# Optimization experiments

Hardware: AMD Instinct MI355X
Metric: run time of the kernel (lower is better)

The kernel has to match this reference:

```python
import jax, jax.numpy as jnp
import numpy as np

THETA_BASE = 10000.0


def rope(x):
    # x: [B, S, D], D even. Interleaved-pair rotary embedding.
    B, S, D = x.shape
    pos = jnp.arange(S, dtype=jnp.float32)                       # [S]
    p = jnp.arange(D // 2, dtype=jnp.float32)                    # p-1 in the torch code
    inv_freq = 1.0 / (THETA_BASE ** (2.0 * p / D))               # [D/2]
    theta = pos[:, None] * inv_freq[None, :]                     # [S, D/2]
    sin_t, cos_t = jnp.sin(theta), jnp.cos(theta)
    x1 = x[..., 0::2]                                            # [B, S, D/2]
    x2 = x[..., 1::2]
    r1 = x1 * cos_t - x2 * sin_t
    r2 = x1 * sin_t + x2 * cos_t
    return jnp.stack((r1, r2), axis=-1).reshape(B, S, D)


def setup_inputs() -> dict:
    key = jax.random.key(0)
    k_x, k_q, k_k, k_v = jax.random.split(key, 4)
    B, S, E, DH = 4, 4096, 1024, 64
    x = jax.random.normal(k_x, (B, S, E), dtype=jnp.float32)
    # causal lower-triangular mask (mask==0 positions are disallowed)
    mask = jnp.tril(jnp.ones((S, S), dtype=jnp.int32))
    W_Q = jax.random.uniform(k_q, (E, DH), dtype=jnp.float32)
    W_K = jax.random.uniform(k_k, (E, DH), dtype=jnp.float32)
    W_V = jax.random.uniform(k_v, (E, DH), dtype=jnp.float32)
    return {"x": x, "mask": mask, "W_Q": W_Q, "W_K": W_K, "W_V": W_V}


def reference(x, mask, W_Q, W_K, W_V):
    d_h = W_Q.shape[1]
    Q = x @ W_Q                                                  # [B, S, d_h]
    K = x @ W_K
    V = x @ W_V
    Q, K = rope(Q), rope(K)
    scores = jnp.einsum('bqd,bkd->bqk', Q, K) / jnp.sqrt(jnp.float32(d_h))
    masked = jnp.where(mask == 0, -jnp.inf, scores)              # broadcast [S,S] -> [B,S,S]
    attn = jax.nn.softmax(masked, axis=-1)
    return jnp.einsum('bqk,bkd->bqd', attn, V)
```

## Files before the change

kernel.cpp:

```cpp
#include <hip/hip_runtime.h>

typedef short short8  __attribute__((ext_vector_type(8)));
typedef short short4v __attribute__((ext_vector_type(4)));
typedef float f32x4   __attribute__((ext_vector_type(4)));
typedef int   i32x4   __attribute__((ext_vector_type(4)));

#define NB 4
#define NS 4096
#define NE 1024
#define ND 64

__device__ __forceinline__ short f2bf(float f) {
    unsigned u = __builtin_bit_cast(unsigned, f);
    u = (u + 0x7FFFu + ((u >> 16) & 1u)) >> 16;
    return (short)u;
}
__device__ __forceinline__ float bf2f(short s) {
    unsigned u = ((unsigned)(unsigned short)s) << 16;
    return __builtin_bit_cast(float, u);
}

__global__ void prep_wt(const float* __restrict__ WQ, const float* __restrict__ WK,
                        const float* __restrict__ WV,
                        short* __restrict__ wtp_hi, short* __restrict__ wtp_lo) {
    int idx = blockIdx.x * 256 + threadIdx.x;
    if (idx >= 192 * NE) return;
    int n = idx >> 10, k = idx & (NE - 1);
    int sel = n >> 6, d = n & 63;
    const float* W = (sel == 0) ? WQ : (sel == 1 ? WK : WV);
    float v = W[k * ND + d];
    if (sel == 0) v *= 0.125f;
    short hi = f2bf(v);
    short lo = f2bf(v - bf2f(hi));
    int off = ((k >> 5) * 12 + (n >> 4)) * 512 + ((k & 31) >> 3) * 128 + (n & 15) * 8 + (k & 7);
    wtp_hi[off] = hi;
    wtp_lo[off] = lo;
}

__global__ __launch_bounds__(256, 2) void proj_rope(
        const float* __restrict__ x,
        const short* __restrict__ wtp_hi, const short* __restrict__ wtp_lo,
        short* __restrict__ qhi, short* __restrict__ qlo,
        short* __restrict__ khi, short* __restrict__ klo,
        short* __restrict__ vtb) {
    __shared__ short Xh[32 * 64], Xl[32 * 64];
    const int tid = threadIdx.x;
    const int w = tid >> 6, lane = tid & 63;
    const int g = lane >> 4, cl = lane & 15;
    const int rb = blockIdx.x << 5;
    const int c0 = w * 48;

    f32x4 acc[2][3];
    #pragma unroll
    for (int i = 0; i < 2; ++i)
        #pragma unroll
        for (int j = 0; j < 3; ++j) acc[i][j] = (f32x4){0.f, 0.f, 0.f, 0.f};

    const int srow = tid >> 3, skc = tid & 7;
    const float* xs0 = x + (size_t)(rb + srow) * NE + (skc << 3);
    const int swoff = srow * 64 + ((skc ^ (srow & 7)) << 3);

    const short* bph = wtp_hi + (size_t)(c0 >> 4) * 512 + (lane << 3);
    const short* bpl = wtp_lo + (size_t)(c0 >> 4) * 512 + (lane << 3);

    float4 xr0, xr1;
    short8 b0[6], b1[6];

#define LOADXR(kk) { xr0 = *(const float4*)(xs0 + (kk)); \
                     xr1 = *(const float4*)(xs0 + (kk) + 4); }
#define LOADB(Bs, kk) {                                                      \
        const int ko = ((kk) >> 5) * 6144;                                   \
        _Pragma("unroll")                                                    \
        for (int ct = 0; ct < 3; ++ct) {                                     \
            Bs[ct * 2]     = *(const short8*)(bph + ko + ct * 512);          \
            Bs[ct * 2 + 1] = *(const short8*)(bpl + ko + ct * 512);          \
        } }
#define HALF(h, Bs) {                                                        \
        _Pragma("unroll")                                                    \
        for (int rt = 0; rt < 2; ++rt) {                                     \
            const int R = (rt << 4) + cl;                                    \
            const int ro = R * 64 + ((((h) * 4 + g) ^ (R & 7)) << 3);        \
            short8 ah = *(const short8*)(Xh + ro);                           \
            short8 al = *(const short8*)(Xl + ro);                           \
            _Pragma("unroll")                                                \
            for (int ct = 0; ct < 3; ++ct) {                                 \
                acc[rt][ct] = __builtin_amdgcn_mfma_f32_16x16x32_bf16(ah, Bs[ct*2],   acc[rt][ct], 0, 0, 0); \
                acc[rt][ct] = __builtin_amdgcn_mfma_f32_16x16x32_bf16(ah, Bs[ct*2+1], acc[rt][ct], 0, 0, 0); \
                acc[rt][ct] = __builtin_amdgcn_mfma_f32_16x16x32_bf16(al, Bs[ct*2],   acc[rt][ct], 0, 0, 0); \
            }                                                                \
        } }

    LOADXR(0);
    LOADB(b0, 0);

    #pragma unroll 1
    for (int k0 = 0; k0 < NE; k0 += 64) {
        short8 h8, l8;
        {
            float vv[8] = {xr0.x, xr0.y, xr0.z, xr0.w, xr1.x, xr1.y, xr1.z, xr1.w};
            #pragma unroll
            for (int q = 0; q < 8; ++q) {
                short h = f2bf(vv[q]);
                h8[q] = h;
                l8[q] = f2bf(vv[q] - bf2f(h));
            }
        }
        __syncthreads();
        *(short8*)(Xh + swoff) = h8;
        *(short8*)(Xl + swoff) = l8;
        if (k0 + 64 < NE) LOADXR(k0 + 64);
        LOADB(b1, k0 + 32);
        __syncthreads();
        HALF(0, b0);
        if (k0 + 64 < NE) LOADB(b0, k0 + 64);
        HALF(1, b1);
    }
#undef LOADXR
#undef LOADB
#undef HALF

    #pragma unroll
    for (int rt = 0; rt < 2; ++rt) {
        #pragma unroll
        for (int ct = 0; ct < 3; ++ct) {
            int c = c0 + (ct << 4) + cl;
            #pragma unroll
            for (int r = 0; r < 4; ++r) {
                int row = rb + (rt << 4) + (g << 2) + r;
                int s = row & (NS - 1);
                int b = row >> 12;
                float val = acc[rt][ct][r];
                if (c < 128) {
                    int d = c & 63;
                    int p = d >> 1;
                    float freq = exp2f(-(float)p * 0.41524101186091903f);
                    float theta = (float)s * freq;
                    float sn = sinf(theta), cs = cosf(theta);
                    float partner = __shfl_xor(val, 1);
                    float rot = (c & 1) ? fmaf(partner, sn, val * cs)
                                        : fmaf(-partner, sn, val * cs);
                    short hi = f2bf(rot);
                    short lo = f2bf(rot - bf2f(hi));
                    int off = row * ND + d;
                    if (c < 64) { qhi[off] = hi; qlo[off] = lo; }
                    else        { khi[off] = hi; klo[off] = lo; }
                } else {
                    int d = c - 128;
                    vtb[(b << 18) + ((s >> 5) << 11) + (d << 5) + (s & 31)] = f2bf(val);
                }
            }
        }
    }
}

__global__ __launch_bounds__(256) void attn_fused(
        const short* __restrict__ qhi, const short* __restrict__ qlo,
        const short* __restrict__ khi, const short* __restrict__ klo,
        const short* __restrict__ vtb, float* __restrict__ outp) {
    __shared__ char sm[49152];
    const int tid = threadIdx.x;
    const int lane = tid & 63, w = tid >> 6;
    const int g = lane >> 4, cl = lane & 15;
    const int bid = blockIdx.x;
    const int b = (bid >> 1) & 3;
    const int t = 255 - (((bid >> 3) << 1) | (bid & 1));
    const int qw = t << 4;
    const int rowb = b << 12;

    char* SW  = sm + w * 12288;
    short* Ps = (short*)(SW + 4096);

    short8 qh[2], ql[2];
    #pragma unroll
    for (int ks = 0; ks < 2; ++ks) {
        int off = ((rowb + qw + cl) << 6) + (ks << 5) + (g << 3);
        qh[ks] = *(const short8*)(qhi + off);
        ql[ks] = *(const short8*)(qlo + off);
    }

    f32x4 o[4];
    #pragma unroll
    for (int i = 0; i < 4; ++i) o[i] = (f32x4){0.f, 0.f, 0.f, 0.f};
    float m = -1e38f, lsp = 0.f;

    const int nkv = (t >> 1) + 1;
    const short* kpB = khi + (rowb << 6);
    const short* lpB = klo + (rowb << 6);
    const short* vpB = vtb + (b << 18);

    i32x4 stK[4], stL[4], stV[4];
#define ISSUE(jj) {                                                          \
        const short* kp = kpB + ((jj) << 11);                                \
        const short* lp = lpB + ((jj) << 11);                                \
        const short* vp = vpB + ((jj) << 11);                                \
        _Pragma("unroll")                                                    \
        for (int i = 0; i < 4; ++i) {                                        \
            stK[i] = *(const i32x4*)(kp + (lane << 3) + (i << 9));           \
            stL[i] = *(const i32x4*)(lp + (lane << 3) + (i << 9));           \
            stV[i] = *(const i32x4*)(vp + (lane << 3) + (i << 9));           \
        } }

    if (w < nkv) {
        ISSUE(w);
        #pragma unroll 1
        for (int j = w; j < nkv; j += 4) {
            #pragma unroll
            for (int i = 0; i < 4; ++i) {
                int c = lane + (i << 6);
                int kr = c >> 3, kc = c & 7;
                int koff = (kr << 7) + ((kc ^ (kr & 7)) << 4);
                *(i32x4*)(SW + koff) = stK[i];
                *(i32x4*)(SW + 4096 + koff) = stL[i];
                int vr = c >> 2, vc = c & 3;
                *(i32x4*)(SW + 8192 + (vr << 6) + ((vc ^ (vr & 3)) << 4)) = stV[i];
            }
            int jn = j + 4;
            if (jn < nkv) ISSUE(jn);

            f32x4 sc[2];
            #pragma unroll
            for (int ci = 0; ci < 2; ++ci) {
                const int rbase = ((ci << 4) + cl) << 7;
                const int sw = (cl & 7) << 4;
                short8 kh0 = *(short8*)(SW + rbase + (((g << 4)     ) ^ sw));
                short8 kh1 = *(short8*)(SW + rbase + (((g << 4) + 64) ^ sw));
                short8 kl0 = *(short8*)(SW + 4096 + rbase + (((g << 4)     ) ^ sw));
                short8 kl1 = *(short8*)(SW + 4096 + rbase + (((g << 4) + 64) ^ sw));
                f32x4 s = (f32x4){0.f, 0.f, 0.f, 0.f};
                s = __builtin_amdgcn_mfma_f32_16x16x32_bf16(kh0, qh[0], s, 0, 0, 0);
                s = __builtin_amdgcn_mfma_f32_16x16x32_bf16(kh1, qh[1], s, 0, 0, 0);
                s = __builtin_amdgcn_mfma_f32_16x16x32_bf16(kh0, ql[0], s, 0, 0, 0);
                s = __builtin_amdgcn_mfma_f32_16x16x32_bf16(kh1, ql[1], s, 0, 0, 0);
                s = __builtin_amdgcn_mfma_f32_16x16x32_bf16(kl0, qh[0], s, 0, 0, 0);
                s = __builtin_amdgcn_mfma_f32_16x16x32_bf16(kl1, qh[1], s, 0, 0, 0);
                sc[ci] = s;
            }
            if (j == nkv - 1) {
                #pragma unroll
                for (int ci = 0; ci < 2; ++ci)
                    #pragma unroll
                    for (int r = 0; r < 4; ++r)
                        if ((j << 5) + (ci << 4) + (g << 2) + r > qw + cl) sc[ci][r] = -1e30f;
            }
            float pm = fmaxf(fmaxf(fmaxf(sc[0][0], sc[0][1]), fmaxf(sc[0][2], sc[0][3])),
                             fmaxf(fmaxf(sc[1][0], sc[1][1]), fmaxf(sc[1][2], sc[1][3])));
            pm = fmaxf(pm, __shfl_xor(pm, 16));
            pm = fmaxf(pm, __shfl_xor(pm, 32));
            const float mo = m;
            m = fmaxf(m, pm);
            const float rs = __expf(mo - m);
            float psum = 0.f;
            #pragma unroll
            for (int ci = 0; ci < 2; ++ci) {
                float p0 = __expf(sc[ci][0] - m), p1 = __expf(sc[ci][1] - m);
                float p2 = __expf(sc[ci][2] - m), p3 = __expf(sc[ci][3] - m);
                psum += (p0 + p1) + (p2 + p3);
                short4v pk;
                pk[0] = f2bf(p0); pk[1] = f2bf(p1); pk[2] = f2bf(p2); pk[3] = f2bf(p3);
                *(short4v*)(Ps + cl * 40 + (ci << 4) + (g << 2)) = pk;
            }
            lsp = lsp * rs + psum;
            if (__any(m > mo)) {
                float rs4[4];
                #pragma unroll
                for (int r = 0; r < 4; ++r) rs4[r] = __shfl(rs, (g << 2) + r);
                #pragma unroll
                for (int dt = 0; dt < 4; ++dt)
                    #pragma unroll
                    for (int r = 0; r < 4; ++r) o[dt][r] *= rs4[r];
            }
            short8 pa = *(short8*)(Ps + cl * 40 + (g << 3));
            #pragma unroll
            for (int dt = 0; dt < 4; ++dt) {
                int vrow = (dt << 4) + cl;
                short8 vf = *(short8*)(SW + 8192 + (vrow << 6)
                                        + (((g << 4)) ^ ((vrow & 3) << 4)));
                o[dt] = __builtin_amdgcn_mfma_f32_16x16x32_bf16(pa, vf, o[dt], 0, 0, 0);
            }
        }
    }
#undef ISSUE

    {
        float* Co = (float*)SW;
        #pragma unroll
        for (int dt = 0; dt < 4; ++dt)
            #pragma unroll
            for (int r = 0; r < 4; ++r)
                Co[((g << 2) + r) * 66 + (dt << 4) + cl] = o[dt][r];
        lsp += __shfl_xor(lsp, 16);
        lsp += __shfl_xor(lsp, 32);
        if (g == 0) {
            *(float*)(SW + 4224 + (cl << 2)) = m;
            *(float*)(SW + 4288 + (cl << 2)) = lsp;
        }
    }
    __syncthreads();

    if (w == 0) {
        #pragma unroll
        for (int r = 0; r < 4; ++r) {
            const int row = (g << 2) + r;
            float mv[4], lv[4];
            #pragma unroll
            for (int v = 0; v < 4; ++v) {
                mv[v] = *(const float*)(sm + v * 12288 + 4224 + (row << 2));
                lv[v] = *(const float*)(sm + v * 12288 + 4288 + (row << 2));
            }
            float M = fmaxf(fmaxf(mv[0], mv[1]), fmaxf(mv[2], mv[3]));
            float e[4];
            float L = 0.f;
            #pragma unroll
            for (int v = 0; v < 4; ++v) { e[v] = __expf(mv[v] - M); L += lv[v] * e[v]; }
            float inv = 1.f / L;
            #pragma unroll
            for (int dt = 0; dt < 4; ++dt) {
                int d = (dt << 4) + cl;
                float O = 0.f;
                #pragma unroll
                for (int v = 0; v < 4; ++v)
                    O += ((const float*)(sm + v * 12288))[row * 66 + d] * e[v];
                outp[(rowb + qw + row) * ND + d] = O * inv;
            }
        }
    }
}

extern "C" void kernel_launch(void* const* d_in, const int* in_sizes, int n_in,
                              void* d_out, int out_size, void* d_ws, size_t ws_size,
                              hipStream_t stream) {
    const float* x  = (const float*)d_in[0];
    const float* WQ = (const float*)d_in[2];
    const float* WK = (const float*)d_in[3];
    const float* WV = (const float*)d_in[4];

    const size_t need = 786432u + 4u * 2097152u + 2097152u;
    if (ws_size < need) return;

    char* ws = (char*)d_ws;
    short* wtph = (short*)(ws);
    short* wtpl = (short*)(ws + 393216);
    short* qhi  = (short*)(ws + 786432);
    short* qlo  = (short*)(ws + 786432 + 1 * 2097152);
    short* khi  = (short*)(ws + 786432 + 2 * 2097152);
    short* klo  = (short*)(ws + 786432 + 3 * 2097152);
    short* vtb  = (short*)(ws + 786432 + 4 * 2097152);

    prep_wt<<<768, 256, 0, stream>>>(WQ, WK, WV, wtph, wtpl);
    proj_rope<<<512, 256, 0, stream>>>(x, wtph, wtpl, qhi, qlo, khi, klo, vtb);
    attn_fused<<<1024, 256, 0, stream>>>(qhi, qlo, khi, klo, vtb, (float*)d_out);
}
```

Baseline: 88.53 us.

## Pre-pack K/V in MFMA fragment layout and load directly into registers

The projection kernel now writes K (hi/lo) and V in a layout that matches the MFMA operand fragments, so the attention kernel loads each lane's fragments straight from global memory into registers. This removes the per-tile LDS staging writes, swizzle and LDS reads. It also shrinks shared memory to the P, output-combine and stats buffers and sets launch bounds to 4 blocks per CU for higher occupancy. In exchange the fragment loads are used directly by MFMAs with less latency hiding, and the next-tile prefetch is split into separate K and V loads.

```diff
diff --git a/kernel.cpp b/kernel.cpp
--- a/kernel.cpp
+++ b/kernel.cpp
@@ -3,7 +3,6 @@
 typedef short short8  __attribute__((ext_vector_type(8)));
 typedef short short4v __attribute__((ext_vector_type(4)));
 typedef float f32x4   __attribute__((ext_vector_type(4)));
-typedef int   i32x4   __attribute__((ext_vector_type(4)));
 
 #define NB 4
 #define NS 4096
@@ -41,8 +40,8 @@
         const float* __restrict__ x,
         const short* __restrict__ wtp_hi, const short* __restrict__ wtp_lo,
         short* __restrict__ qhi, short* __restrict__ qlo,
-        short* __restrict__ khi, short* __restrict__ klo,
-        short* __restrict__ vtb) {
+        short* __restrict__ kfph, short* __restrict__ kfpl,
+        short* __restrict__ vfp) {
     __shared__ short Xh[32 * 64], Xl[32 * 64];
     const int tid = threadIdx.x;
     const int w = tid >> 6, lane = tid & 63;
@@ -141,23 +140,32 @@
                                         : fmaf(-partner, sn, val * cs);
                     short hi = f2bf(rot);
                     short lo = f2bf(rot - bf2f(hi));
-                    int off = row * ND + d;
-                    if (c < 64) { qhi[off] = hi; qlo[off] = lo; }
-                    else        { khi[off] = hi; klo[off] = lo; }
+                    if (c < 64) {
+                        int off = row * ND + d;
+                        qhi[off] = hi; qlo[off] = lo;
+                    } else {
+                        int off = ((b << 7) + (s >> 5)) * 2048 + ((s >> 4) & 1) * 1024
+                                + (d >> 5) * 512 + (((d >> 3) & 3) * 16 + (s & 15)) * 8 + (d & 7);
+                        kfph[off] = hi; kfpl[off] = lo;
+                    }
                 } else {
                     int d = c - 128;
-                    vtb[(b << 18) + ((s >> 5) << 11) + (d << 5) + (s & 31)] = f2bf(val);
+                    int off = ((b << 7) + (s >> 5)) * 2048 + (d >> 4) * 512
+                            + (((s >> 3) & 3) * 16 + (d & 15)) * 8 + (s & 7);
+                    vfp[off] = f2bf(val);
                 }
             }
         }
     }
 }
 
-__global__ __launch_bounds__(256) void attn_fused(
+__global__ __launch_bounds__(256, 4) void attn_fused(
         const short* __restrict__ qhi, const short* __restrict__ qlo,
-        const short* __restrict__ khi, const short* __restrict__ klo,
-        const short* __restrict__ vtb, float* __restrict__ outp) {
-    __shared__ char sm[49152];
+        const short* __restrict__ kfph, const short* __restrict__ kfpl,
+        const short* __restrict__ vfp, float* __restrict__ outp) {
+    __shared__ short Ps[4][16][40];
+    __shared__ float Co[4][16][66];
+    __shared__ float Cm[4][16], Cls[4][16];
     const int tid = threadIdx.x;
     const int lane = tid & 63, w = tid >> 6;
     const int g = lane >> 4, cl = lane & 15;
@@ -167,9 +175,6 @@
     const int qw = t << 4;
     const int rowb = b << 12;
 
-    char* SW  = sm + w * 12288;
-    short* Ps = (short*)(SW + 4096);
-
     short8 qh[2], ql[2];
     #pragma unroll
     for (int ks = 0; ks < 2; ++ks) {
@@ -184,57 +189,48 @@
     float m = -1e38f, lsp = 0.f;
 
     const int nkv = (t >> 1) + 1;
-    const short* kpB = khi + (rowb << 6);
-    const short* lpB = klo + (rowb << 6);
-    const short* vpB = vtb + (b << 18);
-
-    i32x4 stK[4], stL[4], stV[4];
-#define ISSUE(jj) {                                                          \
-        const short* kp = kpB + ((jj) << 11);                                \
-        const short* lp = lpB + ((jj) << 11);                                \
-        const short* vp = vpB + ((jj) << 11);                                \
+    const short* kbaseh = kfph + (size_t)(b << 7) * 2048 + (lane << 3);
+    const short* kbasel = kfpl + (size_t)(b << 7) * 2048 + (lane << 3);
+    const short* vbase  = vfp  + (size_t)(b << 7) * 2048 + (lane << 3);
+
+    short8 kf[2][4];
+    short8 vf[4];
+
+#define LOADK(jj) {                                                          \
         _Pragma("unroll")                                                    \
-        for (int i = 0; i < 4; ++i) {                                        \
-            stK[i] = *(const i32x4*)(kp + (lane << 3) + (i << 9));           \
-            stL[i] = *(const i32x4*)(lp + (lane << 3) + (i << 9));           \
-            stV[i] = *(const i32x4*)(vp + (lane << 3) + (i << 9));           \
+        for (int ci = 0; ci < 2; ++ci) {                                     \
+            const short* kh = kbaseh + (jj) * 2048 + ci * 1024;              \
+            const short* kl = kbasel + (jj) * 2048 + ci * 1024;              \
+            kf[ci][0] = *(const short8*)(kh);                                \
+            kf[ci][1] = *(const short8*)(kh + 512);                          \
+            kf[ci][2] = *(const short8*)(kl);                                \
+            kf[ci][3] = *(const short8*)(kl + 512);                          \
         } }
+#define LOADV(jj) {                                                          \
+        _Pragma("unroll")                                                    \
+        for (int dt = 0; dt < 4; ++dt)                                       \
+            vf[dt] = *(const short8*)(vbase + (jj) * 2048 + dt * 512);       \
+        }
 
     if (w < nkv) {
-        ISSUE(w);
+        LOADK(w); LOADV(w);
         #pragma unroll 1
         for (int j = w; j < nkv; j += 4) {
-            #pragma unroll
-            for (int i = 0; i < 4; ++i) {
-                int c = lane + (i << 6);
-                int kr = c >> 3, kc = c & 7;
-                int koff = (kr << 7) + ((kc ^ (kr & 7)) << 4);
-                *(i32x4*)(SW + koff) = stK[i];
-                *(i32x4*)(SW + 4096 + koff) = stL[i];
-                int vr = c >> 2, vc = c & 3;
-                *(i32x4*)(SW + 8192 + (vr << 6) + ((vc ^ (vr & 3)) << 4)) = stV[i];
-            }
-            int jn = j + 4;
-            if (jn < nkv) ISSUE(jn);
-
             f32x4 sc[2];
             #pragma unroll
             for (int ci = 0; ci < 2; ++ci) {
-                const int rbase = ((ci << 4) + cl) << 7;
-                const int sw = (cl & 7) << 4;
-                short8 kh0 = *(short8*)(SW + rbase + (((g << 4)     ) ^ sw));
-                short8 kh1 = *(short8*)(SW + rbase + (((g << 4) + 64) ^ sw));
-                short8 kl0 = *(short8*)(SW + 4096 + rbase + (((g << 4)     ) ^ sw));
-                short8 kl1 = *(short8*)(SW + 4096 + rbase + (((g << 4) + 64) ^ sw));
                 f32x4 s = (f32x4){0.f, 0.f, 0.f, 0.f};
-                s = __builtin_amdgcn_mfma_f32_16x16x32_bf16(kh0, qh[0], s, 0, 0, 0);
-                s = __builtin_amdgcn_mfma_f32_16x16x32_bf16(kh1, qh[1], s, 0, 0, 0);
-                s = __builtin_amdgcn_mfma_f32_16x16x32_bf16(kh0, ql[0], s, 0, 0, 0);
-                s = __builtin_amdgcn_mfma_f32_16x16x32_bf16(kh1, ql[1], s, 0, 0, 0);
-                s = __builtin_amdgcn_mfma_f32_16x16x32_bf16(kl0, qh[0], s, 0, 0, 0);
-                s = __builtin_amdgcn_mfma_f32_16x16x32_bf16(kl1, qh[1], s, 0, 0, 0);
+                s = __builtin_amdgcn_mfma_f32_16x16x32_bf16(kf[ci][0], qh[0], s, 0, 0, 0);
+                s = __builtin_amdgcn_mfma_f32_16x16x32_bf16(kf[ci][1], qh[1], s, 0, 0, 0);
+                s = __builtin_amdgcn_mfma_f32_16x16x32_bf16(kf[ci][0], ql[0], s, 0, 0, 0);
+                s = __builtin_amdgcn_mfma_f32_16x16x32_bf16(kf[ci][1], ql[1], s, 0, 0, 0);
+                s = __builtin_amdgcn_mfma_f32_16x16x32_bf16(kf[ci][2], qh[0], s, 0, 0, 0);
+                s = __builtin_amdgcn_mfma_f32_16x16x32_bf16(kf[ci][3], qh[1], s, 0, 0, 0);
                 sc[ci] = s;
             }
+            const int jn = j + 4;
+            if (jn < nkv) LOADK(jn);
+
             if (j == nkv - 1) {
                 #pragma unroll
                 for (int ci = 0; ci < 2; ++ci)
@@ -257,7 +253,7 @@
                 psum += (p0 + p1) + (p2 + p3);
                 short4v pk;
                 pk[0] = f2bf(p0); pk[1] = f2bf(p1); pk[2] = f2bf(p2); pk[3] = f2bf(p3);
-                *(short4v*)(Ps + cl * 40 + (ci << 4) + (g << 2)) = pk;
+                *(short4v*)(&Ps[w][cl][(ci << 4) + (g << 2)]) = pk;
             }
             lsp = lsp * rs + psum;
             if (__any(m > mo)) {
@@ -269,57 +265,40 @@
                     #pragma unroll
                     for (int r = 0; r < 4; ++r) o[dt][r] *= rs4[r];
             }
-            short8 pa = *(short8*)(Ps + cl * 40 + (g << 3));
-            #pragma unroll
-            for (int dt = 0; dt < 4; ++dt) {
-                int vrow = (dt << 4) + cl;
-                short8 vf = *(short8*)(SW + 8192 + (vrow << 6)
-                                        + (((g << 4)) ^ ((vrow & 3) << 4)));
-                o[dt] = __builtin_amdgcn_mfma_f32_16x16x32_bf16(pa, vf, o[dt], 0, 0, 0);
-            }
-        }
-    }
-#undef ISSUE
-
-    {
-        float* Co = (float*)SW;
+            short8 pa = *(short8*)(&Ps[w][cl][g << 3]);
+            #pragma unroll
+            for (int dt = 0; dt < 4; ++dt)
+                o[dt] = __builtin_amdgcn_mfma_f32_16x16x32_bf16(pa, vf[dt], o[dt], 0, 0, 0);
+            if (jn < nkv) LOADV(jn);
+        }
+    }
+#undef LOADK
+#undef LOADV
+
+    lsp += __shfl_xor(lsp, 16);
+    lsp += __shfl_xor(lsp, 32);
+    if (g == 0) { Cm[w][cl] = m; Cls[w][cl] = lsp; }
+    #pragma unroll
+    for (int dt = 0; dt < 4; ++dt)
         #pragma unroll
-        for (int dt = 0; dt < 4; ++dt)
-            #pragma unroll
-            for (int r = 0; r < 4; ++r)
-                Co[((g << 2) + r) * 66 + (dt << 4) + cl] = o[dt][r];
-        lsp += __shfl_xor(lsp, 16);
-        lsp += __shfl_xor(lsp, 32);
-        if (g == 0) {
-            *(float*)(SW + 4224 + (cl << 2)) = m;
-            *(float*)(SW + 4288 + (cl << 2)) = lsp;
-        }
-    }
+        for (int r = 0; r < 4; ++r)
+            Co[w][(g << 2) + r][(dt << 4) + cl] = o[dt][r];
     __syncthreads();
 
     if (w == 0) {
         #pragma unroll
         for (int r = 0; r < 4; ++r) {
             const int row = (g << 2) + r;
-            float mv[4], lv[4];
-            #pragma unroll
-            for (int v = 0; v < 4; ++v) {
-                mv[v] = *(const float*)(sm + v * 12288 + 4224 + (row << 2));
-                lv[v] = *(const float*)(sm + v * 12288 + 4288 + (row << 2));
-            }
-            float M = fmaxf(fmaxf(mv[0], mv[1]), fmaxf(mv[2], mv[3]));
-            float e[4];
-            float L = 0.f;
-            #pragma unroll
-            for (int v = 0; v < 4; ++v) { e[v] = __expf(mv[v] - M); L += lv[v] * e[v]; }
+            float M = fmaxf(fmaxf(Cm[0][row], Cm[1][row]), fmaxf(Cm[2][row], Cm[3][row]));
+            float e0 = __expf(Cm[0][row] - M), e1 = __expf(Cm[1][row] - M);
+            float e2 = __expf(Cm[2][row] - M), e3 = __expf(Cm[3][row] - M);
+            float L = Cls[0][row] * e0 + Cls[1][row] * e1 + Cls[2][row] * e2 + Cls[3][row] * e3;
             float inv = 1.f / L;
             #pragma unroll
             for (int dt = 0; dt < 4; ++dt) {
                 int d = (dt << 4) + cl;
-                float O = 0.f;
-                #pragma unroll
-                for (int v = 0; v < 4; ++v)
-                    O += ((const float*)(sm + v * 12288))[row * 66 + d] * e[v];
+                float O = Co[0][row][d] * e0 + Co[1][row][d] * e1
+                        + Co[2][row][d] * e2 + Co[3][row][d] * e3;
                 outp[(rowb + qw + row) * ND + d] = O * inv;
             }
         }
@@ -334,7 +313,7 @@
     const float* WK = (const float*)d_in[3];
     const float* WV = (const float*)d_in[4];
 
-    const size_t need = 786432u + 4u * 2097152u + 2097152u;
+    const size_t need = 786432u + 5u * 2097152u;
     if (ws_size < need) return;
 
     char* ws = (char*)d_ws;
@@ -342,11 +321,11 @@
     short* wtpl = (short*)(ws + 393216);
     short* qhi  = (short*)(ws + 786432);
     short* qlo  = (short*)(ws + 786432 + 1 * 2097152);
-    short* khi  = (short*)(ws + 786432 + 2 * 2097152);
-    short* klo  = (short*)(ws + 786432 + 3 * 2097152);
-    short* vtb  = (short*)(ws + 786432 + 4 * 2097152);
+    short* kfph = (short*)(ws + 786432 + 2 * 2097152);
+    short* kfpl = (short*)(ws + 786432 + 3 * 2097152);
+    short* vfp  = (short*)(ws + 786432 + 4 * 2097152);
 
     prep_wt<<<768, 256, 0, stream>>>(WQ, WK, WV, wtph, wtpl);
-    proj_rope<<<512, 256, 0, stream>>>(x, wtph, wtpl, qhi, qlo, khi, klo, vtb);
-    attn_fused<<<1024, 256, 0, stream>>>(qhi, qlo, khi, klo, vtb, (float*)d_out);
-}
+    proj_rope<<<512, 256, 0, stream>>>(x, wtph, wtpl, qhi, qlo, kfph, kfpl, vfp);
+    attn_fused<<<1024, 256, 0, stream>>>(qhi, qlo, kfph, kfpl, vfp, (float*)d_out);
+}
```

Result: faster. 81.26 us (-8.2%).
